# Kernel optimization log

Measured on AMD Instinct MI355X. Metric: run time of the kernel, lower is better.

Reference implementation:

```python
import jax, jax.numpy as jnp
import numpy as np

H = 16        # num_heads
HD = 64       # head_dim
D = 1024      # hidden_size
SPAN = 32     # pos_ebd_size (= position_buckets)
MAXREL = 128  # max_relative_positions


def make_log_bucket_position(rel_pos, bucket_size, max_position):
    # DeBERTa-v2 log bucketing (int in, int out)
    sign = jnp.sign(rel_pos).astype(jnp.float32)
    mid = bucket_size // 2
    abs_pos = jnp.where((rel_pos < mid) & (rel_pos > -mid), mid - 1, jnp.abs(rel_pos))
    log_pos = jnp.ceil(
        jnp.log(abs_pos.astype(jnp.float32) / mid)
        / np.float32(np.log((max_position - 1) / mid)) * (mid - 1)
    ) + mid
    return jnp.where(abs_pos <= mid, rel_pos, (log_pos * sign).astype(jnp.int32))


def layernorm(x, g, b, eps=1e-5):
    mu = jnp.mean(x, axis=-1, keepdims=True)
    var = jnp.mean((x - mu) ** 2, axis=-1, keepdims=True)
    return (x - mu) * jax.lax.rsqrt(var + eps) * g + b


def setup_inputs() -> dict:
    key = jax.random.key(0)
    ks = jax.random.split(key, 16)
    B, Tq, Tk = 4, 1024, 1024
    s = 0.02
    f32 = jnp.float32
    return {
        "query_states": jax.random.normal(ks[0], (B, Tq, D), f32),
        "key_value_states": jax.random.normal(ks[1], (B, Tk, D), f32),
        "attention_mask": jnp.zeros((B, Tk), jnp.bool_),
        "Wq": jax.random.normal(ks[2], (D, D), f32) * s, "bq": jnp.zeros((D,), f32),
        "Wk": jax.random.normal(ks[3], (D, D), f32) * s, "bk": jnp.zeros((D,), f32),
        "Wv": jax.random.normal(ks[4], (D, D), f32) * s, "bv": jnp.zeros((D,), f32),
        "Wo": jax.random.normal(ks[5], (D, D), f32) * s, "bo": jnp.zeros((D,), f32),
        "rel_emb": jax.random.normal(ks[6], (2 * SPAN, D), f32) * s,
        "ln_g": jnp.ones((D,), f32), "ln_b": jnp.zeros((D,), f32),
        "Wpk": jax.random.normal(ks[7], (D, D), f32) * s, "bpk": jnp.zeros((D,), f32),
        "Wpq": jax.random.normal(ks[8], (D, D), f32) * s, "bpq": jnp.zeros((D,), f32),
    }


def reference(query_states, key_value_states, attention_mask,
              Wq, bq, Wk, bk, Wv, bv, Wo, bo,
              rel_emb, ln_g, ln_b, Wpk, bpk, Wpq, bpq):
    B, Tq, _ = query_states.shape
    Tk = key_value_states.shape[1]

    # project + split heads: [B, H, T, HD]
    q = (query_states @ Wq + bq).reshape(B, Tq, H, HD).transpose(0, 2, 1, 3)
    k = (key_value_states @ Wk + bk).reshape(B, Tk, H, HD).transpose(0, 2, 1, 3)
    v = (key_value_states @ Wv + bv).reshape(B, Tk, H, HD).transpose(0, 2, 1, 3)

    # content-to-content, scale_factor = 1 + c2p + p2c = 3
    scale = jnp.sqrt(jnp.float32(HD * 3))
    scores = jnp.einsum('bhqd,bhkd->bhqk', q, k) / scale

    # normalized relative embeddings and positional projections: [H, 2S, HD]
    rel = layernorm(rel_emb, ln_g, ln_b)
    pos_k = (rel @ Wpk + bpk).reshape(2 * SPAN, H, HD).transpose(1, 0, 2)
    pos_q = (rel @ Wpq + bpq).reshape(2 * SPAN, H, HD).transpose(1, 0, 2)

    # bucketed relative positions [Tq, Tk]
    rel_pos = make_log_bucket_position(
        jnp.arange(Tq)[:, None] - jnp.arange(Tk)[None, :], SPAN, MAXREL)

    bias_scale = jnp.sqrt(jnp.float32(HD * 2))
    # c2p: [B,H,Tq,2S] gathered to [B,H,Tq,Tk]
    c2p = jnp.einsum('bhqd,hsd->bhqs', q, pos_k)
    c2p_idx = jnp.clip(rel_pos + SPAN, 0, 2 * SPAN - 1)
    c2p_bias = jnp.take_along_axis(c2p, c2p_idx[None, None], axis=-1)
    # p2c: [B,H,Tk,2S] gathered to [B,H,Tk,Tq], then transposed (requires Tq==Tk)
    p2c = jnp.einsum('bhkd,hsd->bhks', k, pos_q)
    p2c_idx = jnp.clip(-rel_pos + SPAN, 0, 2 * SPAN - 1)
    p2c_bias = jnp.take_along_axis(p2c, p2c_idx[None, None], axis=-1).transpose(0, 1, 3, 2)

    scores = scores + (c2p_bias + p2c_bias) / bias_scale
    scores = jnp.where(attention_mask[:, None, None, :], -jnp.inf, scores)
    probs = jax.nn.softmax(scores.astype(jnp.float32), axis=-1).astype(q.dtype)

    ctx = jnp.einsum('bhqk,bhkd->bhqd', probs, v)
    ctx = ctx.transpose(0, 2, 1, 3).reshape(B, Tq, H * HD)
    return ctx @ Wo + bo
```

## Files before the change

### kernel.cpp

```cpp
#include <hip/hip_runtime.h>
#include <cstdint>
#include <math.h>

typedef unsigned short us;
typedef __attribute__((ext_vector_type(8))) __bf16 bf16x8;
typedef __attribute__((ext_vector_type(8))) unsigned short ushort8;
typedef __attribute__((ext_vector_type(4))) float f32x4;

__device__ __forceinline__ us f2bf(float x){
  union { float f; unsigned int u; } v; v.f = x;
  unsigned int r = v.u + 0x7FFFu + ((v.u >> 16) & 1u);
  return (us)(r >> 16);
}
__device__ __forceinline__ float b2f(us u){
  union { unsigned int u; float f; } v; v.u = ((unsigned int)u) << 16; return v.f;
}
__device__ __forceinline__ void split2(float x, us& hi, us& lo){
  hi = f2bf(x); lo = f2bf(x - b2f(hi));
}
__device__ __forceinline__ f32x4 fzero(){ f32x4 v; v.x=0.f; v.y=0.f; v.z=0.f; v.w=0.f; return v; }
__device__ __forceinline__ f32x4 mfma16(bf16x8 a, bf16x8 b, f32x4 c){
  return __builtin_amdgcn_mfma_f32_16x16x32_bf16(a, b, c, 0, 0, 0);
}
__device__ __forceinline__ void gload_lds16(const void* g, void* l){
  __builtin_amdgcn_global_load_lds(
      (const __attribute__((address_space(1))) unsigned int*)(uintptr_t)g,
      (__attribute__((address_space(3))) unsigned int*)(uintptr_t)l,
      16, 0, 0);
}

#define QS2 (0.07216878364870322f * 1.4426950408889634f)
#define BS  (0.08838834764831845f * 1.4426950408889634f)

__global__ __launch_bounds__(256) void k_prep(const float* __restrict__ xq,
                                              const float* __restrict__ xkv,
                                              const float* __restrict__ w0, const float* __restrict__ w1,
                                              const float* __restrict__ w2, const float* __restrict__ w3,
                                              const float* __restrict__ w4, const float* __restrict__ w5,
                                              const float* __restrict__ rel,
                                              const float* __restrict__ g, const float* __restrict__ bLN,
                                              us* __restrict__ qhi, us* __restrict__ kvhi,
                                              us* __restrict__ wt, us* __restrict__ reln_hi,
                                              signed char* __restrict__ idxt)
{
  __shared__ float tile[32][33];
  __shared__ float sm[8];
  const int bid = blockIdx.x, t = threadIdx.x;

  if (bid < 8192){
    int i = bid * 256 + t;
    const float* src; us* dh;
    if (i < 1048576){ src = xq  + (size_t)i*4;           dh = qhi  + (size_t)i*4; }
    else            { src = xkv + (size_t)(i-1048576)*4; dh = kvhi + (size_t)(i-1048576)*4; }
    f32x4 v = *(const f32x4*)src;
    dh[0]=f2bf(v.x); dh[1]=f2bf(v.y); dh[2]=f2bf(v.z); dh[3]=f2bf(v.w);
    return;
  }
  if (bid < 14336){
    int rem = bid - 8192;
    int z = rem >> 10, r2 = rem & 1023;
    const float* W = (z==0)?w0:(z==1)?w1:(z==2)?w2:(z==3)?w3:(z==4)?w4:w5;
    us* dst_hi = wt + (size_t)z * 2097152;
    us* dst_lo = dst_hi + 1048576;
    bool wlo = (z == 2) || (z == 5);
    int n0 = (r2 & 31) * 32, k0 = (r2 >> 5) * 32;
    int c = t & 31, r = t >> 5;
#pragma unroll
    for (int i = 0; i < 4; i++)
      tile[r + i*8][c] = W[(size_t)(k0 + r + i*8)*1024 + n0 + c];
    __syncthreads();
#pragma unroll
    for (int i = 0; i < 4; i++){
      int nn = r + i*8;
      us h,l; split2(tile[c][nn], h, l);
      dst_hi[(size_t)(n0 + nn)*1024 + k0 + c] = h;
      if (wlo) dst_lo[(size_t)(n0 + nn)*1024 + k0 + c] = l;
    }
    return;
  }
  if (bid < 14400){
    int row = bid - 14336;
    const float* x = rel + (size_t)row * 1024;
    float v[4]; float s = 0.f, ss = 0.f;
#pragma unroll
    for (int i=0;i<4;i++){ v[i] = x[t + 256*i]; s += v[i]; ss += v[i]*v[i]; }
    for (int o=32;o;o>>=1){ s += __shfl_xor(s,o); ss += __shfl_xor(ss,o); }
    int w = t >> 6;
    if ((t & 63) == 0){ sm[w] = s; sm[4+w] = ss; }
    __syncthreads();
    s  = sm[0]+sm[1]+sm[2]+sm[3];
    ss = sm[4]+sm[5]+sm[6]+sm[7];
    float mu  = s  * (1.0f/1024.0f);
    float var = ss * (1.0f/1024.0f) - mu*mu;
    float rs  = rsqrtf(var + 1e-5f);
#pragma unroll
    for (int i=0;i<4;i++){
      int cc = t + 256*i;
      reln_hi[(size_t)row*1024 + cc] = f2bf((v[i]-mu)*rs*g[cc] + bLN[cc]);
    }
    return;
  }
  {
    int i = (bid - 14400) * 256 + t;
    if (i >= 2052) return;
    int d = i - 1023;
    int ad = d < 0 ? -d : d;
    int abspos = (d < 16 && d > -16) ? 15 : ad;
    int bucket;
    if (abspos <= 16) bucket = d;
    else {
      float num = (float)log((double)abspos * 0.0625);
      float den = (float)log(7.9375);
      float lp = ceilf(num / den * 15.0f) + 16.0f;
      bucket = (int)lp * (d > 0 ? 1 : -1);
    }
    int s = bucket + 32;
    s = s < 0 ? 0 : (s > 63 ? 63 : s);
    idxt[i] = (signed char)s;
  }
}

__global__ __launch_bounds__(256) void k_qkvp(const us* __restrict__ Xq, const us* __restrict__ Xkv,
                                              const us* __restrict__ wt,
                                              const float* __restrict__ bq, const float* __restrict__ bk,
                                              const float* __restrict__ bv,
                                              const us* __restrict__ reln_hi,
                                              const float* __restrict__ bpk, const float* __restrict__ bpq,
                                              us* __restrict__ qbuf, us* __restrict__ kbuf,
                                              us* __restrict__ vtb,
                                              us* __restrict__ posk_hi, us* __restrict__ posq_hi)
{
  __shared__ __align__(16) us a_lds[2][4096];
  __shared__ __align__(16) us b_lds[2][4096];
  const int bid = blockIdx.x;
  const int t = threadIdx.x, w = t >> 6, lane = t & 63, lg = lane >> 4, li = lane & 15;

  if (bid >= 768){
    int wg2 = bid - 768;
    int ntile = wg2 & 15, z = wg2 >> 4;
    const us* W_hi = wt + (size_t)(3 + z) * 2097152;
    const float* bias = z ? bpq : bpk;
    us* out_hi = z ? posq_hi : posk_hi;
    f32x4 acc[4];
#pragma unroll
    for (int i=0;i<4;i++) acc[i] = fzero();
    int srow = w*16 + li;
    for (int kt = 0; kt < 32; kt++){
      int k0 = kt*32 + lg*8;
      bf16x8 a = *(const bf16x8*)(reln_hi + (size_t)srow*1024 + k0);
#pragma unroll
      for (int nf=0; nf<4; nf++){
        int n = ntile*64 + nf*16 + li;
        bf16x8 b = *(const bf16x8*)(W_hi + (size_t)n*1024 + k0);
        acc[nf] = mfma16(a, b, acc[nf]);
      }
    }
#pragma unroll
    for (int nf=0;nf<4;nf++){
      int n = ntile*64 + nf*16 + li;
      float bn = bias[n];
      int h = n >> 6, hd = n & 63;
#pragma unroll
      for (int j=0;j<4;j++){
        int s = w*16 + lg*4 + j;
        out_hi[(size_t)h*4096 + s*64 + hd] = f2bf(acc[nf][j] + bn);
      }
    }
    return;
  }

  int cls = bid >> 8;
  int u = bid & 255;
  int tile = (u & 7) * 32 + (u >> 3);
  int mt = tile >> 3, nt = tile & 7;
  int m0 = mt * 128, n0 = nt * 128;
  const us* A  = (cls == 0) ? Xq : Xkv;
  const us* Bh = wt + (size_t)cls * 2097152;
  const us* Bl = Bh + 1048576;
  const float* bias = (cls==0) ? bq : (cls==1) ? bk : bv;
  const int NKT = (cls == 2) ? 64 : 32;
  int wm = w >> 1, wn = w & 1;
  f32x4 acc[4][4];
#pragma unroll
  for (int i=0;i<4;i++)
#pragma unroll
    for (int j=0;j<4;j++) acc[i][j] = fzero();

  auto stage = [&](int buf, int kt){
    int seg = kt >> 5, k0 = (kt & 31) * 32;
    const us* Bp = seg ? Bl : Bh;
#pragma unroll
    for (int c = 0; c < 2; c++){
      int slot = c*256 + t;
      int g = slot ^ ((slot >> 3) & 7);
      int r = g >> 2, kc = g & 3;
      gload_lds16(A  + (size_t)(m0 + r)*1024 + k0 + kc*8, (char*)&a_lds[buf][0] + slot*16);
      gload_lds16(Bp + (size_t)(n0 + r)*1024 + k0 + kc*8, (char*)&b_lds[buf][0] + slot*16);
    }
  };

  stage(0, 0);
  __syncthreads();
  int buf = 0;
  for (int kt = 0; kt < NKT; kt++){
    if (kt + 1 < NKT) stage(buf ^ 1, kt + 1);
    bf16x8 af[4], bfv[4];
#pragma unroll
    for (int mi=0;mi<4;mi++){
      int r = wm*64 + mi*16 + li;
      int s = (r*4 + lg); s ^= ((s >> 3) & 7);
      af[mi] = *(const bf16x8*)((char*)&a_lds[buf][0] + s*16);
    }
#pragma unroll
    for (int ni=0;ni<4;ni++){
      int r = wn*64 + ni*16 + li;
      int s = (r*4 + lg); s ^= ((s >> 3) & 7);
      bfv[ni] = *(const bf16x8*)((char*)&b_lds[buf][0] + s*16);
    }
#pragma unroll
    for (int mi=0;mi<4;mi++)
#pragma unroll
      for (int ni=0;ni<4;ni++)
        acc[mi][ni] = mfma16(af[mi], bfv[ni], acc[mi][ni]);
    __syncthreads();
    buf ^= 1;
  }

#pragma unroll
  for (int ni=0;ni<4;ni++){
    int n = n0 + wn*64 + ni*16 + li;
    float bn = bias[n];
    int hh = n >> 6, hd = n & 63;
#pragma unroll
    for (int mi=0;mi<4;mi++){
      int mb = m0 + wm*64 + mi*16 + lg*4;
#pragma unroll
      for (int j=0;j<4;j++){
        int m = mb + j;
        float val = acc[mi][ni][j] + bn;
        int bb = m >> 10, tp = m & 1023;
        if (cls == 2)
          vtb[(((size_t)(bb*16 + hh))*64 + hd)*1024 + tp] = f2bf(val);
        else {
          us* out = cls ? kbuf : qbuf;
          out[(((size_t)(bb*16 + hh))*1024 + tp)*64 + hd] = f2bf(val);
        }
      }
    }
  }
}

__global__ __launch_bounds__(256, 2) void k_gemmo(const us* __restrict__ A_hi, const us* __restrict__ A_lo,
                                                  const us* __restrict__ B_hi, const us* __restrict__ B_lo,
                                                  const float* __restrict__ bias,
                                                  float* __restrict__ out_f)
{
  __shared__ __align__(16) us a_lds[2][4096];
  __shared__ __align__(16) us b_lds[2][2048];
  int bid = blockIdx.x;
  int wg = (bid & 7) * 64 + (bid >> 3);
  int mt = wg >> 4, nt = wg & 15;
  int m0 = mt * 128, n0 = nt * 64;
  int t = threadIdx.x, w = t >> 6, lane = t & 63, lg = lane >> 4, li = lane & 15;
  int wm = w >> 1, wn = w & 1;
  f32x4 acc[4][2];
#pragma unroll
  for (int i=0;i<4;i++){ acc[i][0]=fzero(); acc[i][1]=fzero(); }

  auto stage = [&](int buf, int kt){
    int seg = kt >> 5, k0 = (kt & 31) * 32;
    const us* Ap = (seg == 2) ? A_lo : A_hi;
    const us* Bp = (seg == 1) ? B_lo : B_hi;
#pragma unroll
    for (int c = 0; c < 2; c++){
      int slot = c*256 + t;
      int g = slot ^ ((slot >> 3) & 7);
      int r = g >> 2, kc = g & 3;
      gload_lds16(Ap + (size_t)(m0 + r)*1024 + k0 + kc*8, (char*)&a_lds[buf][0] + slot*16);
    }
    {
      int slot = t;
      int g = slot ^ ((slot >> 3) & 7);
      int r = g >> 2, kc = g & 3;
      gload_lds16(Bp + (size_t)(n0 + r)*1024 + k0 + kc*8, (char*)&b_lds[buf][0] + slot*16);
    }
  };

  stage(0, 0);
  __syncthreads();
  int buf = 0;
  for (int kt = 0; kt < 96; kt++){
    if (kt + 1 < 96) stage(buf ^ 1, kt + 1);
    bf16x8 af[4], bfv[2];
#pragma unroll
    for (int mi=0;mi<4;mi++){
      int r = wm*64 + mi*16 + li;
      int s = (r*4 + lg); s ^= ((s >> 3) & 7);
      af[mi] = *(const bf16x8*)((char*)&a_lds[buf][0] + s*16);
    }
#pragma unroll
    for (int ni=0;ni<2;ni++){
      int r = wn*32 + ni*16 + li;
      int s = (r*4 + lg); s ^= ((s >> 3) & 7);
      bfv[ni] = *(const bf16x8*)((char*)&b_lds[buf][0] + s*16);
    }
#pragma unroll
    for (int mi=0;mi<4;mi++)
#pragma unroll
      for (int ni=0;ni<2;ni++)
        acc[mi][ni] = mfma16(af[mi], bfv[ni], acc[mi][ni]);
    __syncthreads();
    buf ^= 1;
  }

#pragma unroll
  for (int ni=0;ni<2;ni++){
    int n = n0 + wn*32 + ni*16 + li;
    float bn = bias[n];
#pragma unroll
    for (int mi=0;mi<4;mi++){
      int mb = m0 + wm*64 + mi*16 + lg*4;
#pragma unroll
      for (int j=0;j<4;j++)
        out_f[(size_t)(mb + j)*1024 + n] = acc[mi][ni][j] + bn;
    }
  }
}

__global__ __launch_bounds__(256) void k_cp(const us* __restrict__ q_hi,
                                            const us* __restrict__ k_hi,
                                            const us* __restrict__ pk_hi,
                                            const us* __restrict__ pq_hi,
                                            us* __restrict__ c2p, us* __restrict__ p2c)
{
  int qt = blockIdx.x, bh = blockIdx.y, z = blockIdx.z;
  const us* X_hi = z ? k_hi : q_hi;
  const us* P_hi = z ? pq_hi : pk_hi;
  us* out = z ? p2c : c2p;
  int h = bh & 15;
  int t = threadIdx.x, w = t >> 6, lane = t & 63, lg = lane >> 4, li = lane & 15;
  f32x4 acc[4];
#pragma unroll
  for (int i=0;i<4;i++) acc[i] = fzero();
  size_t row = (size_t)bh*1024 + qt*64 + w*16 + li;
#pragma unroll
  for (int kk=0;kk<2;kk++){
    int k = kk*32 + lg*8;
    bf16x8 ah = *(const bf16x8*)(X_hi + row*64 + k);
#pragma unroll
    for (int nf=0;nf<4;nf++){
      int s = nf*16 + li;
      bf16x8 bh_ = *(const bf16x8*)(P_hi + (size_t)h*4096 + s*64 + k);
      acc[nf] = mfma16(ah, bh_, acc[nf]);
    }
  }
  size_t obase = ((size_t)bh*1024 + qt*64 + w*16 + lg*4) * 64;
#pragma unroll
  for (int nf=0;nf<4;nf++)
#pragma unroll
    for (int j=0;j<4;j++)
      out[obase + (size_t)j*64 + nf*16 + li] = f2bf(acc[nf][j] * BS);
}

__global__ __launch_bounds__(512) void k_attn(const us* __restrict__ qhi,
                                              const us* __restrict__ khi,
                                              const us* __restrict__ vhi,
                                              const us* __restrict__ c2p, const us* __restrict__ p2c,
                                              const signed char* __restrict__ idxt,
                                              const unsigned char* __restrict__ mask,
                                              us* __restrict__ ctx_hi, us* __restrict__ ctx_lo)
{
  __shared__ __align__(16) us khi_lds[4096], vhi_lds[4096];
  __shared__ __align__(16) us c2p_lds[128*72], p2c_lds[64*72];
  __shared__ __align__(16) us p_lds[8][1024];
  __shared__ signed char idx_lds[2048];

  const int qt = blockIdx.x, bh = blockIdx.y;
  const int b = bh >> 4, h = bh & 15;
  const int t = threadIdx.x, w = t >> 6, lane = t & 63, lg = lane >> 4, li = lane & 15;
  const int q0 = qt * 128;

  for (int i = t; i < 2047; i += 512) idx_lds[i] = idxt[i];
  {
    const us* src = c2p + ((size_t)bh*1024 + q0) * 64;
#pragma unroll
    for (int c = 0; c < 2; c++){
      int f = c*512 + t, r = f >> 3, kc = f & 7;
      *(ushort8*)&c2p_lds[r*72 + kc*8] = *(const ushort8*)(src + r*64 + kc*8);
    }
  }
  bf16x8 qfh[2];
  {
    const us* qph = qhi + ((size_t)bh*1024 + q0 + w*16 + li)*64 + lg*8;
    qfh[0] = *(const bf16x8*)(qph); qfh[1] = *(const bf16x8*)(qph + 32);
  }
  __syncthreads();
  float cq0[4], cq63[4];
#pragma unroll
  for (int j=0;j<4;j++){
    int qloc = w*16 + lg*4 + j;
    cq0[j]  = b2f(c2p_lds[qloc*72 + 0]);
    cq63[j] = b2f(c2p_lds[qloc*72 + 63]);
  }

  float lrow[4];
  f32x4 accO[4];
#pragma unroll
  for (int j=0;j<4;j++){ lrow[j] = 0.f; accO[j] = fzero(); }
  const unsigned char* mptr = mask + b*1024;

  for (int kt = 0; kt < 16; kt++){
    const int k0 = kt * 64;
    const bool far = (q0 - k0 >= 192) || (k0 - q0 >= 256);
    __syncthreads();
    {
      int r = t >> 3, kc = t & 7;
      *(ushort8*)&khi_lds[r*64 + ((kc ^ (r & 7))*8)] =
          *(const ushort8*)(khi + ((size_t)bh*1024 + k0 + r)*64 + kc*8);
      *(ushort8*)&vhi_lds[r*64 + ((kc ^ (r & 7))*8)] =
          *(const ushort8*)(vhi + ((size_t)bh*64 + r)*1024 + k0 + kc*8);
      if (!far)
        *(ushort8*)&p2c_lds[r*72 + kc*8] =
            *(const ushort8*)(p2c + ((size_t)bh*1024 + k0 + r)*64 + kc*8);
    }
    __syncthreads();

    f32x4 sfr[4];
#pragma unroll
    for (int nf=0;nf<4;nf++) sfr[nf] = fzero();
#pragma unroll
    for (int kk=0; kk<2; kk++){
      int kc = kk*4 + lg;
#pragma unroll
      for (int nf=0; nf<4; nf++){
        int r = nf*16 + li;
        bf16x8 bh_ = *(const bf16x8*)&khi_lds[r*64 + ((kc ^ (r & 7))*8)];
        sfr[nf] = mfma16(qfh[kk], bh_, sfr[nf]);
      }
    }
    us* pl = &p_lds[w][0];
    if (far){
      const int cidx = (q0 > k0) ? 63 : 0;
      float cq[4];
#pragma unroll
      for (int j=0;j<4;j++) cq[j] = (q0 > k0) ? cq63[j] : cq0[j];
#pragma unroll
      for (int nf=0; nf<4; nf++){
        int kloc = nf*16 + li;
        bool mk = mptr[k0 + kloc] != 0;
        float ck = b2f(p2c[((size_t)bh*1024 + k0 + kloc)*64 + cidx]);
        int col = kloc;
#pragma unroll
        for (int j=0;j<4;j++){
          float p = mk ? 0.f : exp2f(fmaf(sfr[nf][j], QS2, cq[j] + ck));
          lrow[j] += p;
          int row = lg*4 + j;
          pl[row*64 + ((col & 7) | ((((col >> 3) ^ (row & 7))) << 3))] = f2bf(p);
        }
      }
    } else {
#pragma unroll
      for (int nf=0; nf<4; nf++){
        int kloc = nf*16 + li;
        bool mk = mptr[k0 + kloc] != 0;
        int col = kloc;
#pragma unroll
        for (int j=0;j<4;j++){
          int qloc = w*16 + lg*4 + j;
          int d = (q0 + qloc) - (k0 + kloc);
          int idx = (int)idx_lds[d + 1023];
          float s2 = fmaf(sfr[nf][j], QS2,
                          b2f(c2p_lds[qloc*72 + idx]) + b2f(p2c_lds[kloc*72 + idx]));
          float p = mk ? 0.f : exp2f(s2);
          lrow[j] += p;
          int row = lg*4 + j;
          pl[row*64 + ((col & 7) | ((((col >> 3) ^ (row & 7))) << 3))] = f2bf(p);
        }
      }
    }
#pragma unroll
    for (int kk=0;kk<2;kk++){
      int kc = kk*4 + lg;
      bf16x8 af = *(const bf16x8*)((char*)pl + li*128 + ((kc ^ (li & 7)) * 16));
#pragma unroll
      for (int nf=0;nf<4;nf++){
        int r = nf*16 + li;
        bf16x8 bh_ = *(const bf16x8*)&vhi_lds[r*64 + ((kc ^ (r & 7))*8)];
        accO[nf] = mfma16(af, bh_, accO[nf]);
      }
    }
  }

  for (int o=1;o<16;o<<=1)
#pragma unroll
    for (int j=0;j<4;j++)
      lrow[j] += __shfl_xor(lrow[j], o);
#pragma unroll
  for (int nf=0;nf<4;nf++)
#pragma unroll
    for (int j=0;j<4;j++){
      int qloc = w*16 + lg*4 + j;
      float o = accO[nf][j] / lrow[j];
      size_t idx = ((size_t)(b*1024 + q0 + qloc))*1024 + h*64 + nf*16 + li;
      us hh,ll; split2(o,hh,ll);
      ctx_hi[idx] = hh; ctx_lo[idx] = ll;
    }
}

extern "C" void kernel_launch(void* const* d_in, const int* in_sizes, int n_in,
                              void* d_out, int out_size, void* d_ws, size_t ws_size,
                              hipStream_t stream)
{
  (void)in_sizes; (void)n_in; (void)out_size; (void)ws_size;
  const float* query = (const float*)d_in[0];
  const float* kvst  = (const float*)d_in[1];
  const unsigned char* mask = (const unsigned char*)d_in[2];
  const float* Wq = (const float*)d_in[3];  const float* bq = (const float*)d_in[4];
  const float* Wk = (const float*)d_in[5];  const float* bk = (const float*)d_in[6];
  const float* Wv = (const float*)d_in[7];  const float* bv = (const float*)d_in[8];
  const float* Wo = (const float*)d_in[9];  const float* bo = (const float*)d_in[10];
  const float* rel = (const float*)d_in[11];
  const float* lng = (const float*)d_in[12]; const float* lnb = (const float*)d_in[13];
  const float* Wpk = (const float*)d_in[14]; const float* bpk = (const float*)d_in[15];
  const float* Wpq = (const float*)d_in[16]; const float* bpq = (const float*)d_in[17];

  char* ws = (char*)d_ws;
  const size_t MB = 1024*1024;
  us* Xq_hi  = (us*)(ws + 0);
  us* p2c    = (us*)(ws + 8*MB);
  us* Xkv_hi = (us*)(ws + 16*MB);
  us* c2p    = (us*)(ws + 16*MB);
  us* vtb_hi = (us*)(ws + 24*MB);
  us* Wt     = (us*)(ws + 32*MB);
  us* ctx_hi = (us*)(ws + 32*MB);
  us* ctx_lo = (us*)(ws + 40*MB);
  us* reln_hi = (us*)(ws + 56*MB);
  us* posk_hi = (us*)(ws + 56*MB + 256*1024);
  us* posq_hi = (us*)(ws + 56*MB + 512*1024);
  signed char* idxt = (signed char*)(ws + 56*MB + 768*1024);
  us* qbuf_hi = (us*)(ws + 57*MB);
  us* kbuf_hi = (us*)(ws + 65*MB);

  k_prep<<<14409, 256, 0, stream>>>(query, kvst, Wq, Wk, Wv, Wpk, Wpq, Wo,
                                    rel, lng, lnb,
                                    Xq_hi, Xkv_hi, Wt, reln_hi, idxt);

  k_qkvp<<<800, 256, 0, stream>>>(Xq_hi, Xkv_hi, Wt, bq, bk, bv,
                                  reln_hi, bpk, bpq,
                                  qbuf_hi, kbuf_hi, vtb_hi, posk_hi, posq_hi);

  k_cp<<<dim3(16,64,2), 256, 0, stream>>>(qbuf_hi, kbuf_hi, posk_hi, posq_hi, c2p, p2c);

  k_attn<<<dim3(8,64), 512, 0, stream>>>(qbuf_hi, kbuf_hi, vtb_hi,
                                         c2p, p2c, idxt, mask, ctx_hi, ctx_lo);

  k_gemmo<<<512, 256, 0, stream>>>(ctx_hi, ctx_lo, Wt + 5*2097152, Wt + 5*2097152 + 1048576, bo, (float*)d_out);
}
```

Measured before the change: 201.5 us.

## Split V projection K-loop into two blocks and reduce partials in k_cp

The V projection previously ran 64 K-steps (hi and lo weight halves) in one block, making those 256 blocks twice as long as the Q/K blocks and leaving a tail. It now runs as two sets of 256 blocks, each covering one weight half and writing fp32 partials. A new z=2 slice of k_cp sums the partials, adds the bias and converts to bf16 in the transposed V layout. This balances block work and adds parallelism, at the cost of extra fp32 traffic (two 16MB partial buffers written and read back) and a reshuffled workspace layout.

```diff
diff --git a/kernel.cpp b/kernel.cpp
--- a/kernel.cpp
+++ b/kernel.cpp
@@ -123,11 +123,10 @@
 __global__ __launch_bounds__(256) void k_qkvp(const us* __restrict__ Xq, const us* __restrict__ Xkv,
                                               const us* __restrict__ wt,
                                               const float* __restrict__ bq, const float* __restrict__ bk,
-                                              const float* __restrict__ bv,
                                               const us* __restrict__ reln_hi,
                                               const float* __restrict__ bpk, const float* __restrict__ bpq,
                                               us* __restrict__ qbuf, us* __restrict__ kbuf,
-                                              us* __restrict__ vtb,
+                                              float* __restrict__ vtb_p0, float* __restrict__ vtb_p1,
                                               us* __restrict__ posk_hi, us* __restrict__ posq_hi)
 {
   __shared__ __align__(16) us a_lds[2][4096];
@@ -135,8 +134,8 @@
   const int bid = blockIdx.x;
   const int t = threadIdx.x, w = t >> 6, lane = t & 63, lg = lane >> 4, li = lane & 15;
 
-  if (bid >= 768){
-    int wg2 = bid - 768;
+  if (bid >= 1024){
+    int wg2 = bid - 1024;
     int ntile = wg2 & 15, z = wg2 >> 4;
     const us* W_hi = wt + (size_t)(3 + z) * 2097152;
     const float* bias = z ? bpq : bpk;
@@ -174,11 +173,9 @@
   int tile = (u & 7) * 32 + (u >> 3);
   int mt = tile >> 3, nt = tile & 7;
   int m0 = mt * 128, n0 = nt * 128;
-  const us* A  = (cls == 0) ? Xq : Xkv;
-  const us* Bh = wt + (size_t)cls * 2097152;
-  const us* Bl = Bh + 1048576;
-  const float* bias = (cls==0) ? bq : (cls==1) ? bk : bv;
-  const int NKT = (cls == 2) ? 64 : 32;
+  const us* A = (cls == 0) ? Xq : Xkv;
+  const us* Bbase = wt + (size_t)(cls < 2 ? cls : 2) * 2097152;
+  const us* Bp = (cls == 3) ? Bbase + 1048576 : Bbase;
   int wm = w >> 1, wn = w & 1;
   f32x4 acc[4][4];
 #pragma unroll
@@ -187,8 +184,7 @@
     for (int j=0;j<4;j++) acc[i][j] = fzero();
 
   auto stage = [&](int buf, int kt){
-    int seg = kt >> 5, k0 = (kt & 31) * 32;
-    const us* Bp = seg ? Bl : Bh;
+    int k0 = kt * 32;
 #pragma unroll
     for (int c = 0; c < 2; c++){
       int slot = c*256 + t;
@@ -202,8 +198,8 @@
   stage(0, 0);
   __syncthreads();
   int buf = 0;
-  for (int kt = 0; kt < NKT; kt++){
-    if (kt + 1 < NKT) stage(buf ^ 1, kt + 1);
+  for (int kt = 0; kt < 32; kt++){
+    if (kt + 1 < 32) stage(buf ^ 1, kt + 1);
     bf16x8 af[4], bfv[4];
 #pragma unroll
     for (int mi=0;mi<4;mi++){
@@ -229,7 +225,7 @@
 #pragma unroll
   for (int ni=0;ni<4;ni++){
     int n = n0 + wn*64 + ni*16 + li;
-    float bn = bias[n];
+    float bn = (cls == 0) ? bq[n] : (cls == 1) ? bk[n] : 0.f;
     int hh = n >> 6, hd = n & 63;
 #pragma unroll
     for (int mi=0;mi<4;mi++){
@@ -239,9 +235,10 @@
         int m = mb + j;
         float val = acc[mi][ni][j] + bn;
         int bb = m >> 10, tp = m & 1023;
-        if (cls == 2)
-          vtb[(((size_t)(bb*16 + hh))*64 + hd)*1024 + tp] = f2bf(val);
-        else {
+        if (cls >= 2){
+          float* dst = (cls == 2) ? vtb_p0 : vtb_p1;
+          dst[(((size_t)(bb*16 + hh))*64 + hd)*1024 + tp] = val;
+        } else {
           us* out = cls ? kbuf : qbuf;
           out[(((size_t)(bb*16 + hh))*1024 + tp)*64 + hd] = f2bf(val);
         }
@@ -331,14 +328,38 @@
                                             const us* __restrict__ k_hi,
                                             const us* __restrict__ pk_hi,
                                             const us* __restrict__ pq_hi,
-                                            us* __restrict__ c2p, us* __restrict__ p2c)
+                                            const float* __restrict__ vtb_p0,
+                                            const float* __restrict__ vtb_p1,
+                                            const float* __restrict__ bv,
+                                            us* __restrict__ c2p, us* __restrict__ p2c,
+                                            us* __restrict__ vtb)
 {
   int qt = blockIdx.x, bh = blockIdx.y, z = blockIdx.z;
+  int t = threadIdx.x;
+  if (z == 2){
+    int bx = qt + (bh << 4);
+    size_t base = (size_t)bx*4096 + t*16;
+    int n = ((int)(base >> 16) & 15) * 64 + ((int)(base >> 10) & 63);
+    float bn = bv[n];
+    us outv[16];
+#pragma unroll
+    for (int c = 0; c < 4; c++){
+      f32x4 a = *(const f32x4*)(vtb_p0 + base + c*4);
+      f32x4 b = *(const f32x4*)(vtb_p1 + base + c*4);
+      outv[c*4+0] = f2bf(a.x + b.x + bn);
+      outv[c*4+1] = f2bf(a.y + b.y + bn);
+      outv[c*4+2] = f2bf(a.z + b.z + bn);
+      outv[c*4+3] = f2bf(a.w + b.w + bn);
+    }
+    *(ushort8*)(vtb + base)     = *(ushort8*)&outv[0];
+    *(ushort8*)(vtb + base + 8) = *(ushort8*)&outv[8];
+    return;
+  }
   const us* X_hi = z ? k_hi : q_hi;
   const us* P_hi = z ? pq_hi : pk_hi;
   us* out = z ? p2c : c2p;
   int h = bh & 15;
-  int t = threadIdx.x, w = t >> 6, lane = t & 63, lg = lane >> 4, li = lane & 15;
+  int w = t >> 6, lane = t & 63, lg = lane >> 4, li = lane & 15;
   f32x4 acc[4];
 #pragma unroll
   for (int i=0;i<4;i++) acc[i] = fzero();
@@ -526,32 +547,35 @@
 
   char* ws = (char*)d_ws;
   const size_t MB = 1024*1024;
-  us* Xq_hi  = (us*)(ws + 0);
-  us* p2c    = (us*)(ws + 8*MB);
-  us* Xkv_hi = (us*)(ws + 16*MB);
-  us* c2p    = (us*)(ws + 16*MB);
-  us* vtb_hi = (us*)(ws + 24*MB);
-  us* Wt     = (us*)(ws + 32*MB);
-  us* ctx_hi = (us*)(ws + 32*MB);
-  us* ctx_lo = (us*)(ws + 40*MB);
-  us* reln_hi = (us*)(ws + 56*MB);
-  us* posk_hi = (us*)(ws + 56*MB + 256*1024);
-  us* posq_hi = (us*)(ws + 56*MB + 512*1024);
-  signed char* idxt = (signed char*)(ws + 56*MB + 768*1024);
-  us* qbuf_hi = (us*)(ws + 57*MB);
-  us* kbuf_hi = (us*)(ws + 65*MB);
+  us*    Xq_hi   = (us*)(ws + 0);
+  us*    c2p     = (us*)(ws + 0);
+  us*    Xkv_hi  = (us*)(ws + 8*MB);
+  us*    p2c     = (us*)(ws + 8*MB);
+  us*    Wt      = (us*)(ws + 16*MB);
+  us*    vtb     = (us*)(ws + 16*MB);
+  us*    reln_hi = (us*)(ws + 40*MB);
+  us*    posk_hi = (us*)(ws + 40*MB + 256*1024);
+  us*    posq_hi = (us*)(ws + 40*MB + 512*1024);
+  signed char* idxt = (signed char*)(ws + 40*MB + 768*1024);
+  us*    qbuf_hi = (us*)(ws + 41*MB);
+  us*    kbuf_hi = (us*)(ws + 49*MB);
+  float* vtb_p0  = (float*)(ws + 57*MB);
+  us*    ctx_hi  = (us*)(ws + 57*MB);
+  us*    ctx_lo  = (us*)(ws + 65*MB);
+  float* vtb_p1  = (float*)(ws + 73*MB);
 
   k_prep<<<14409, 256, 0, stream>>>(query, kvst, Wq, Wk, Wv, Wpk, Wpq, Wo,
                                     rel, lng, lnb,
                                     Xq_hi, Xkv_hi, Wt, reln_hi, idxt);
 
-  k_qkvp<<<800, 256, 0, stream>>>(Xq_hi, Xkv_hi, Wt, bq, bk, bv,
-                                  reln_hi, bpk, bpq,
-                                  qbuf_hi, kbuf_hi, vtb_hi, posk_hi, posq_hi);
-
-  k_cp<<<dim3(16,64,2), 256, 0, stream>>>(qbuf_hi, kbuf_hi, posk_hi, posq_hi, c2p, p2c);
-
-  k_attn<<<dim3(8,64), 512, 0, stream>>>(qbuf_hi, kbuf_hi, vtb_hi,
+  k_qkvp<<<1056, 256, 0, stream>>>(Xq_hi, Xkv_hi, Wt, bq, bk,
+                                   reln_hi, bpk, bpq,
+                                   qbuf_hi, kbuf_hi, vtb_p0, vtb_p1, posk_hi, posq_hi);
+
+  k_cp<<<dim3(16,64,3), 256, 0, stream>>>(qbuf_hi, kbuf_hi, posk_hi, posq_hi,
+                                          vtb_p0, vtb_p1, bv, c2p, p2c, vtb);
+
+  k_attn<<<dim3(8,64), 512, 0, stream>>>(qbuf_hi, kbuf_hi, vtb,
                                          c2p, p2c, idxt, mask, ctx_hi, ctx_lo);
 
   k_gemmo<<<512, 256, 0, stream>>>(ctx_hi, ctx_lo, Wt + 5*2097152, Wt + 5*2097152 + 1048576, bo, (float*)d_out);
```

Result: slower. 213.0 us (+5.7%).
